# Kernel optimization log

Hardware: AMD Instinct MI355X
Metric: run time of the kernel (lower is better)

## Reference

```python
import jax, jax.numpy as jnp
import numpy as np

B, S, E, H = 2, 2048, 1024, 16
D = E // H  # head_dim = 64


def setup_inputs() -> dict:
    key = jax.random.key(0)
    ks = jax.random.split(key, 6)
    scale = 1.0 / np.sqrt(E)
    x = jax.random.normal(ks[0], (B, S, E), dtype=jnp.float32)
    mask = jnp.ones((B, S), dtype=jnp.int32)
    Wqkv = jax.random.normal(ks[1], (E, 3 * E), dtype=jnp.float32) * scale
    bqkv = jax.random.normal(ks[2], (3 * E,), dtype=jnp.float32) * 0.01
    Wout = jax.random.normal(ks[3], (E, E), dtype=jnp.float32) * scale
    bout = jax.random.normal(ks[4], (E,), dtype=jnp.float32) * 0.01
    return {"x": x, "mask": mask, "Wqkv": Wqkv, "bqkv": bqkv, "Wout": Wout, "bout": bout}


def reference(x, mask, Wqkv, bqkv, Wout, bout):
    Bn, Sn, En = x.shape
    qkv = x @ Wqkv + bqkv                      # [B,S,3E]
    qkv = qkv.reshape(Bn, Sn, 3, H, D)
    qkv = jnp.transpose(qkv, (2, 0, 3, 1, 4))  # [3,B,H,S,D]
    q, k, v = qkv[0], qkv[1], qkv[2]
    scores = jnp.einsum('bhqd,bhkd->bhqk', q, k) / np.sqrt(D).astype(np.float32)
    m = mask[:, None, None, :]                 # [B,1,1,S]
    scores = jnp.where(m == 0, jnp.float32(-jnp.inf), scores)
    attn = jax.nn.softmax(scores, axis=-1)
    out = jnp.einsum('bhqk,bhkd->bhqd', attn, v)  # [B,H,S,D]
    out = jnp.transpose(out, (0, 2, 1, 3)).reshape(Bn, Sn, En)
    return out @ Wout + bout
```

## Files before the change

### kernel.cpp

```cpp
#include <hip/hip_runtime.h>


typedef __attribute__((ext_vector_type(8))) short short8;
typedef __attribute__((ext_vector_type(4))) float floatx4;
typedef unsigned short ushort_t;

static __device__ __forceinline__ ushort_t f2bf(float f) {
    unsigned u = __float_as_uint(f);
    u += 0x7fffu + ((u >> 16) & 1u);
    return (ushort_t)(u >> 16);
}
static __device__ __forceinline__ float bf2f(ushort_t h) {
    return __uint_as_float(((unsigned)h) << 16);
}
#if __has_builtin(__builtin_amdgcn_cvt_pk_bf16_f32)
typedef __attribute__((ext_vector_type(2))) __bf16 bf16x2_t;
static __device__ __forceinline__ unsigned pack2bf(float a, float b) {
    bf16x2_t r = __builtin_amdgcn_cvt_pk_bf16_f32(a, b);
    return __builtin_bit_cast(unsigned, r);
}
#else
static __device__ __forceinline__ unsigned pack2bf(float a, float b) {
    return (unsigned)f2bf(a) | ((unsigned)f2bf(b) << 16);
}
#endif
static __device__ __forceinline__ float hexp2(float x) {
    return __builtin_amdgcn_exp2f(x);
}
static __device__ __forceinline__ void gload16(const void* g, void* l) {
    __builtin_amdgcn_global_load_lds(
        (const __attribute__((address_space(1))) unsigned int*)g,
        (__attribute__((address_space(3))) unsigned int*)l, 16, 0, 0);
}

__global__ __launch_bounds__(256) void prep(
    const float* __restrict__ x, ushort_t* __restrict__ xb,
    const float* __restrict__ Wqkv, ushort_t* __restrict__ wqT,
    const float* __restrict__ Wout, ushort_t* __restrict__ woT,
    const int* __restrict__ mask, float* __restrict__ maddg)
{
    __shared__ float tile[32][33];
    const int bk = blockIdx.x;
    const int t = threadIdx.x;
    if (bk < 4096) {
        int i = bk * 256 + t;
        float4 v = ((const float4*)x)[i];
        uint2 o;
        o.x = pack2bf(v.x, v.y);
        o.y = pack2bf(v.z, v.w);
        ((uint2*)xb)[i] = o;
        return;
    }
    if (bk < 8192) {
        const float* W; ushort_t* WT; int K, N, id;
        if (bk < 7168) { W = Wqkv; WT = wqT; K = 1024; N = 3072; id = bk - 4096;
                         int nb = (id % 96) * 32, kb = (id / 96) * 32;
                         const int r = t >> 3, c4 = (t & 7) * 4;
                         float4 v = *(const float4*)&W[(size_t)(kb + r) * N + nb + c4];
                         tile[r][c4+0]=v.x; tile[r][c4+1]=v.y; tile[r][c4+2]=v.z; tile[r][c4+3]=v.w;
                         __syncthreads();
                         uint2 o;
                         o.x = pack2bf(tile[c4+0][r], tile[c4+1][r]);
                         o.y = pack2bf(tile[c4+2][r], tile[c4+3][r]);
                         ((uint2*)WT)[((size_t)(nb + r) * K + kb + c4) >> 2] = o;
        } else {         W = Wout; WT = woT; K = 1024; N = 1024; id = bk - 7168;
                         int nb = (id % 32) * 32, kb = (id / 32) * 32;
                         const int r = t >> 3, c4 = (t & 7) * 4;
                         float4 v = *(const float4*)&W[(size_t)(kb + r) * N + nb + c4];
                         tile[r][c4+0]=v.x; tile[r][c4+1]=v.y; tile[r][c4+2]=v.z; tile[r][c4+3]=v.w;
                         __syncthreads();
                         uint2 o;
                         o.x = pack2bf(tile[c4+0][r], tile[c4+1][r]);
                         o.y = pack2bf(tile[c4+2][r], tile[c4+3][r]);
                         ((uint2*)WT)[((size_t)(nb + r) * K + kb + c4) >> 2] = o;
        }
        return;
    }
    {
        int i = (bk - 8192) * 256 + t;
        maddg[i] = (mask[i] ? 0.f : -1e30f) - 24.0f;
    }
}

__global__ __launch_bounds__(256, 3) void gemm_qkv(
    const ushort_t* __restrict__ A, const ushort_t* __restrict__ B,
    const float* __restrict__ bias, ushort_t* __restrict__ qkvb,
    ushort_t* __restrict__ vtg)
{
    const int K = 1024;
    __shared__ ushort_t Ah[128][32], Bh[128][32];
    __shared__ ushort_t Tb[64][136];
    const int bn = blockIdx.x * 128, bm = blockIdx.y * 128;
    const int t = threadIdx.x, w = t >> 6, lane = t & 63;
    const int l15 = lane & 15, quad = lane >> 4;
    const int wm = w >> 1, wn = w & 1;

    const int srow = w * 32 + (lane >> 2);
    const int skp  = (lane & 3) ^ ((lane >> 2) & 3);
    const int scol = skp * 8;
    const ushort_t* ga = A + (size_t)(bm + srow) * K + scol;
    const ushort_t* gb = B + (size_t)(bn + srow) * K + scol;
    const size_t rstep = (size_t)16 * K;
    const int fcol = ((quad ^ (l15 & 3)) * 8);

    floatx4 acc[4][4];
    #pragma unroll
    for (int mt = 0; mt < 4; ++mt)
        #pragma unroll
        for (int nt = 0; nt < 4; ++nt) acc[mt][nt] = (floatx4){0.f, 0.f, 0.f, 0.f};

    for (int k0 = 0; k0 < K; k0 += 32) {
        #pragma unroll
        for (int i = 0; i < 2; ++i) {
            gload16(ga + i * rstep + k0, &Ah[w * 32 + i * 16][0]);
            gload16(gb + i * rstep + k0, &Bh[w * 32 + i * 16][0]);
        }
        __syncthreads();
        short8 ah[4], bh[4];
        #pragma unroll
        for (int x = 0; x < 4; ++x) {
            ah[x] = *(const short8*)&Ah[wm * 64 + x * 16 + l15][fcol];
            bh[x] = *(const short8*)&Bh[wn * 64 + x * 16 + l15][fcol];
        }
        #pragma unroll
        for (int mt = 0; mt < 4; ++mt)
            #pragma unroll
            for (int nt = 0; nt < 4; ++nt)
                acc[mt][nt] = __builtin_amdgcn_mfma_f32_16x16x32_bf16(ah[mt], bh[nt], acc[mt][nt], 0, 0, 0);
        __syncthreads();
    }

    if (bn < 2048) {
        #pragma unroll
        for (int mt = 0; mt < 4; ++mt)
            #pragma unroll
            for (int r = 0; r < 4; ++r) {
                size_t row = (size_t)(bm + wm * 64 + mt * 16 + quad * 4 + r) * 2048;
                #pragma unroll
                for (int nt = 0; nt < 4; ++nt) {
                    int col = bn + wn * 64 + nt * 16 + l15;
                    qkvb[row + col] = f2bf(acc[mt][nt][r] + bias[col]);
                }
            }
    } else {
        const int h0 = (bn - 2048) >> 6;
        const int b  = bm >> 11, s0 = bm & 2047;
        #pragma unroll
        for (int hh = 0; hh < 2; ++hh) {
            if (wn == hh) {
                #pragma unroll
                for (int mt = 0; mt < 4; ++mt)
                    #pragma unroll
                    for (int nt = 0; nt < 4; ++nt) {
                        int d = nt * 16 + l15;
                        int sb = wm * 64 + mt * 16 + quad * 4;
                        float bv = bias[bn + hh * 64 + nt * 16 + l15];
                        uint2 pk;
                        pk.x = pack2bf(acc[mt][nt][0] + bv, acc[mt][nt][1] + bv);
                        pk.y = pack2bf(acc[mt][nt][2] + bv, acc[mt][nt][3] + bv);
                        *(uint2*)&Tb[d][sb] = pk;
                    }
            }
            __syncthreads();
            ushort_t* vbase = vtg + ((size_t)((b * 16 + h0 + hh) * 64)) * 2048 + s0;
            #pragma unroll
            for (int it = 0; it < 4; ++it) {
                int idx = t + it * 256;
                int d = idx >> 4, ch = idx & 15;
                uint4 v = *(const uint4*)&Tb[d][ch * 8];
                *(uint4*)&vbase[(size_t)d * 2048 + ch * 8] = v;
            }
            __syncthreads();
        }
    }
}

__global__ __launch_bounds__(256, 3) void gemm_bf16_f32_64(
    const ushort_t* __restrict__ A, const ushort_t* __restrict__ B,
    const float* __restrict__ bias, float* __restrict__ C,
    int M, int N, int K)
{
    __shared__ ushort_t Ah[64][32], Bh[128][32];
    const int bn = blockIdx.x * 128, bm = blockIdx.y * 64;
    const int t = threadIdx.x, w = t >> 6, lane = t & 63;
    const int l15 = lane & 15, quad = lane >> 4;
    const int wm = w >> 1, wn = w & 1;

    const int srow = w * 16 + (lane >> 2);
    const int skp  = (lane & 3) ^ ((lane >> 2) & 3);
    const int scol = skp * 8;
    const ushort_t* ga  = A + (size_t)(bm + srow) * K + scol;
    const ushort_t* gb0 = B + (size_t)(bn + srow) * K + scol;
    const ushort_t* gb1 = B + (size_t)(bn + 64 + srow) * K + scol;
    const int fcol = ((quad ^ (l15 & 3)) * 8);

    floatx4 acc[2][4];
    #pragma unroll
    for (int mt = 0; mt < 2; ++mt)
        #pragma unroll
        for (int nt = 0; nt < 4; ++nt) acc[mt][nt] = (floatx4){0.f, 0.f, 0.f, 0.f};

    for (int k0 = 0; k0 < K; k0 += 32) {
        gload16(ga  + k0, &Ah[w * 16][0]);
        gload16(gb0 + k0, &Bh[w * 16][0]);
        gload16(gb1 + k0, &Bh[64 + w * 16][0]);
        __syncthreads();
        short8 ah[2], bh[4];
        #pragma unroll
        for (int x = 0; x < 2; ++x)
            ah[x] = *(const short8*)&Ah[wm * 32 + x * 16 + l15][fcol];
        #pragma unroll
        for (int x = 0; x < 4; ++x)
            bh[x] = *(const short8*)&Bh[wn * 64 + x * 16 + l15][fcol];
        #pragma unroll
        for (int mt = 0; mt < 2; ++mt)
            #pragma unroll
            for (int nt = 0; nt < 4; ++nt)
                acc[mt][nt] = __builtin_amdgcn_mfma_f32_16x16x32_bf16(ah[mt], bh[nt], acc[mt][nt], 0, 0, 0);
        __syncthreads();
    }
    #pragma unroll
    for (int mt = 0; mt < 2; ++mt)
        #pragma unroll
        for (int r = 0; r < 4; ++r) {
            size_t row = (size_t)(bm + wm * 32 + mt * 16 + quad * 4 + r) * N;
            #pragma unroll
            for (int nt = 0; nt < 4; ++nt) {
                int col = bn + wn * 64 + nt * 16 + l15;
                C[row + col] = acc[mt][nt][r] + bias[col];
            }
        }
}

__global__ __launch_bounds__(256, 2) void flash_v6(
    const ushort_t* __restrict__ qkv, const ushort_t* __restrict__ vtg,
    const float* __restrict__ maddg, ushort_t* __restrict__ attn)
{
    __shared__ ushort_t Ks[2][64][64];
    __shared__ ushort_t Vt[2][64][64];
    __shared__ ushort_t Ps[4][2][16][72];
    __shared__ float MaddL[2048];

    const int blk = blockIdx.x;
    const int xcd = blk & 7, rr = blk >> 3;
    const int qi = rr & 15, g = xcd + 8 * (rr >> 4);
    const int b = g >> 4, h = g & 15, q0 = qi * 128;

    const int t = threadIdx.x, wave = t >> 6, lane = t & 63;
    const int l15 = lane & 15, quad = lane >> 4;
    const size_t bS = (size_t)b * 2048;
    const float c1 = 0.125f * 1.44269504088896340736f;

    short8 qf[2][2];
    #pragma unroll
    for (int tt = 0; tt < 2; ++tt) {
        int q = q0 + wave * 32 + tt * 16 + l15;
        const ushort_t* qp = qkv + (bS + q) * 2048 + h * 64;
        qf[tt][0] = *(const short8*)(qp + quad * 8);
        qf[tt][1] = *(const short8*)(qp + 32 + quad * 8);
    }

    const int srow  = wave * 16 + (lane >> 3);
    const int schnk = ((lane & 7) ^ ((lane >> 3) & 7)) * 8;
    const ushort_t* gK = qkv + (bS + srow) * 2048 + 1024 + h * 64 + schnk;
    const ushort_t* gV = vtg + ((size_t)(b * 16 + h) * 64 + srow) * 2048 + schnk;

    gload16(gK,            &Ks[0][wave * 16][0]);
    gload16(gK + 8 * 2048, &Ks[0][wave * 16 + 8][0]);
    gload16(gV,            &Vt[0][wave * 16][0]);
    gload16(gV + 8 * 2048, &Vt[0][wave * 16 + 8][0]);
    {
        const float* gM = maddg + b * 2048 + wave * 512 + lane * 4;
        gload16(gM,       &MaddL[wave * 512]);
        gload16(gM + 256, &MaddL[wave * 512 + 256]);
    }
    __syncthreads();

    floatx4 outacc[2][4];
    float lsum[2] = {0.f, 0.f};
    #pragma unroll
    for (int tt = 0; tt < 2; ++tt)
        #pragma unroll
        for (int dt = 0; dt < 4; ++dt) outacc[tt][dt] = (floatx4){0.f, 0.f, 0.f, 0.f};

    int cur = 0;
    for (int kt = 0; kt < 32; ++kt) {
        const int k0 = kt * 64;
        {
            const int kn = (kt + 1 < 32) ? (kt + 1) * 64 : 0;
            const int nb = cur ^ 1;
            gload16(gK + (size_t)kn * 2048,            &Ks[nb][wave * 16][0]);
            gload16(gK + (size_t)(kn + 8) * 2048,      &Ks[nb][wave * 16 + 8][0]);
            gload16(gV + kn,                           &Vt[nb][wave * 16][0]);
            gload16(gV + kn + 8 * 2048,                &Vt[nb][wave * 16 + 8][0]);
        }

        short8 kf[2][4], vf[2][4];
        #pragma unroll
        for (int kc = 0; kc < 2; ++kc)
            #pragma unroll
            for (int c = 0; c < 4; ++c) {
                int ch = ((kc * 4 + quad) ^ (l15 & 7)) * 8;
                kf[kc][c] = *(const short8*)&Ks[cur][c * 16 + l15][ch];
                vf[kc][c] = *(const short8*)&Vt[cur][c * 16 + l15][ch];
            }
        float4 madd4[4];
        #pragma unroll
        for (int c = 0; c < 4; ++c)
            madd4[c] = *(const float4*)&MaddL[k0 + c * 16 + quad * 4];

        #pragma unroll
        for (int tt = 0; tt < 2; ++tt) {
            floatx4 sc[4];
            #pragma unroll
            for (int c = 0; c < 4; ++c) {
                sc[c] = (floatx4){0.f, 0.f, 0.f, 0.f};
                sc[c] = __builtin_amdgcn_mfma_f32_16x16x32_bf16(kf[0][c], qf[tt][0], sc[c], 0, 0, 0);
                sc[c] = __builtin_amdgcn_mfma_f32_16x16x32_bf16(kf[1][c], qf[tt][1], sc[c], 0, 0, 0);
            }
            #pragma unroll
            for (int c = 0; c < 4; ++c) {
                float p0 = hexp2(fmaf(sc[c][0], c1, madd4[c].x));
                float p1 = hexp2(fmaf(sc[c][1], c1, madd4[c].y));
                float p2 = hexp2(fmaf(sc[c][2], c1, madd4[c].z));
                float p3 = hexp2(fmaf(sc[c][3], c1, madd4[c].w));
                lsum[tt] += (p0 + p1) + (p2 + p3);
                uint2 pk;
                pk.x = pack2bf(p0, p1);
                pk.y = pack2bf(p2, p3);
                *(uint2*)&Ps[wave][tt][l15][c * 16 + quad * 4] = pk;
            }
            short8 pf0 = *(const short8*)&Ps[wave][tt][l15][quad * 8];
            short8 pf1 = *(const short8*)&Ps[wave][tt][l15][32 + quad * 8];
            #pragma unroll
            for (int dt = 0; dt < 4; ++dt) {
                outacc[tt][dt] = __builtin_amdgcn_mfma_f32_16x16x32_bf16(vf[0][dt], pf0, outacc[tt][dt], 0, 0, 0);
                outacc[tt][dt] = __builtin_amdgcn_mfma_f32_16x16x32_bf16(vf[1][dt], pf1, outacc[tt][dt], 0, 0, 0);
            }
        }
        __syncthreads();
        cur ^= 1;
    }

    #pragma unroll
    for (int tt = 0; tt < 2; ++tt) {
        lsum[tt] += __shfl_xor(lsum[tt], 16);
        lsum[tt] += __shfl_xor(lsum[tt], 32);
        float inv = 1.f / lsum[tt];
        int q = q0 + wave * 32 + tt * 16 + l15;
        ushort_t* orow = attn + (bS + q) * 1024 + h * 64;
        #pragma unroll
        for (int dt = 0; dt < 4; ++dt) {
            uint2 pk;
            pk.x = pack2bf(outacc[tt][dt][0] * inv, outacc[tt][dt][1] * inv);
            pk.y = pack2bf(outacc[tt][dt][2] * inv, outacc[tt][dt][3] * inv);
            *(uint2*)&orow[dt * 16 + quad * 4] = pk;
        }
    }
}

extern "C" void kernel_launch(void* const* d_in, const int* in_sizes, int n_in,
                              void* d_out, int out_size, void* d_ws, size_t ws_size,
                              hipStream_t stream) {
    const float* x    = (const float*)d_in[0];
    const int*   mask = (const int*)  d_in[1];
    const float* Wqkv = (const float*)d_in[2];
    const float* bqkv = (const float*)d_in[3];
    const float* Wout = (const float*)d_in[4];
    const float* bout = (const float*)d_in[5];
    float* out = (float*)d_out;

    char* ws = (char*)d_ws;
    ushort_t* xb    = (ushort_t*)(ws);
    ushort_t* wqT   = (ushort_t*)(ws + 8388608);
    ushort_t* qkvb  = (ushort_t*)(ws + 14680064);
    ushort_t* vtg   = (ushort_t*)(ws + 31457280);
    ushort_t* attnb = (ushort_t*)(ws + 39845888);
    ushort_t* woT   = (ushort_t*)(ws + 48234496);
    float*    maddg = (float*)   (ws + 50331648);

    const int M = 4096, E = 1024, N3 = 3072;

    prep<<<dim3(8208), dim3(256), 0, stream>>>(
        x, xb, Wqkv, wqT, Wout, woT, mask, maddg);

    gemm_qkv<<<dim3(N3 / 128, M / 128), dim3(256), 0, stream>>>(
        xb, wqT, bqkv, qkvb, vtg);

    flash_v6<<<dim3(512), dim3(256), 0, stream>>>(qkvb, vtg, maddg, attnb);

    gemm_bf16_f32_64<<<dim3(E / 128, M / 64), dim3(256), 0, stream>>>(
        attnb, woT, bout, out, M, E, E);
}
```

Measured before the change: 201.7 us.

## Feed P directly from registers into 16x16x16 MFMA, drop LDS P staging

```diff
diff --git a/kernel.cpp b/kernel.cpp
--- a/kernel.cpp
+++ b/kernel.cpp
@@ -2,6 +2,7 @@
 
 
 typedef __attribute__((ext_vector_type(8))) short short8;
+typedef __attribute__((ext_vector_type(4))) short short4b;
 typedef __attribute__((ext_vector_type(4))) float floatx4;
 typedef unsigned short ushort_t;
 
@@ -31,6 +32,17 @@
     __builtin_amdgcn_global_load_lds(
         (const __attribute__((address_space(1))) unsigned int*)g,
         (__attribute__((address_space(3))) unsigned int*)l, 16, 0, 0);
+}
+
+static __device__ __forceinline__ floatx4 mfma16(short4b a, short4b b, floatx4 c) {
+#if __has_builtin(__builtin_amdgcn_mfma_f32_16x16x16_bf16)
+    return __builtin_amdgcn_mfma_f32_16x16x16_bf16(a, b, c, 0, 0, 0);
+#elif __has_builtin(__builtin_amdgcn_mfma_f32_16x16x16bf16_1k)
+    return __builtin_amdgcn_mfma_f32_16x16x16bf16_1k(a, b, c, 0, 0, 0);
+#else
+    asm("v_mfma_f32_16x16x16_bf16 %0, %1, %2, %0" : "+v"(c) : "v"(a), "v"(b));
+    return c;
+#endif
 }
 
 __global__ __launch_bounds__(256) void prep(
@@ -232,14 +244,12 @@
         }
 }
 
-__global__ __launch_bounds__(256, 2) void flash_v6(
+__global__ __launch_bounds__(256, 2) void flash_v7(
     const ushort_t* __restrict__ qkv, const ushort_t* __restrict__ vtg,
     const float* __restrict__ maddg, ushort_t* __restrict__ attn)
 {
     __shared__ ushort_t Ks[2][64][64];
     __shared__ ushort_t Vt[2][64][64];
-    __shared__ ushort_t Ps[4][2][16][72];
-    __shared__ float MaddL[2048];
 
     const int blk = blockIdx.x;
     const int xcd = blk & 7, rr = blk >> 3;
@@ -264,16 +274,12 @@
     const int schnk = ((lane & 7) ^ ((lane >> 3) & 7)) * 8;
     const ushort_t* gK = qkv + (bS + srow) * 2048 + 1024 + h * 64 + schnk;
     const ushort_t* gV = vtg + ((size_t)(b * 16 + h) * 64 + srow) * 2048 + schnk;
+    const float* gM = maddg + b * 2048;
 
     gload16(gK,            &Ks[0][wave * 16][0]);
     gload16(gK + 8 * 2048, &Ks[0][wave * 16 + 8][0]);
     gload16(gV,            &Vt[0][wave * 16][0]);
     gload16(gV + 8 * 2048, &Vt[0][wave * 16 + 8][0]);
-    {
-        const float* gM = maddg + b * 2048 + wave * 512 + lane * 4;
-        gload16(gM,       &MaddL[wave * 512]);
-        gload16(gM + 256, &MaddL[wave * 512 + 256]);
-    }
     __syncthreads();
 
     floatx4 outacc[2][4];
@@ -294,20 +300,27 @@
             gload16(gV + kn,                           &Vt[nb][wave * 16][0]);
             gload16(gV + kn + 8 * 2048,                &Vt[nb][wave * 16 + 8][0]);
         }
-
-        short8 kf[2][4], vf[2][4];
+        float4 madd4[4];
+        #pragma unroll
+        for (int c = 0; c < 4; ++c)
+            madd4[c] = *(const float4*)&gM[k0 + c * 16 + quad * 4];
+
+        short8 kf[2][4];
         #pragma unroll
         for (int kc = 0; kc < 2; ++kc)
             #pragma unroll
             for (int c = 0; c < 4; ++c) {
                 int ch = ((kc * 4 + quad) ^ (l15 & 7)) * 8;
                 kf[kc][c] = *(const short8*)&Ks[cur][c * 16 + l15][ch];
-                vf[kc][c] = *(const short8*)&Vt[cur][c * 16 + l15][ch];
-            }
-        float4 madd4[4];
-        #pragma unroll
-        for (int c = 0; c < 4; ++c)
-            madd4[c] = *(const float4*)&MaddL[k0 + c * 16 + quad * 4];
+            }
+        short4b vA[4][4];
+        #pragma unroll
+        for (int c = 0; c < 4; ++c) {
+            const int vby = (((2 * c + (quad >> 1)) ^ (l15 & 7)) * 16 + (quad & 1) * 8);
+            #pragma unroll
+            for (int dt = 0; dt < 4; ++dt)
+                vA[c][dt] = *(const short4b*)((const char*)&Vt[cur][dt * 16 + l15][0] + vby);
+        }
 
         #pragma unroll
         for (int tt = 0; tt < 2; ++tt) {
@@ -325,17 +338,13 @@
                 float p2 = hexp2(fmaf(sc[c][2], c1, madd4[c].z));
                 float p3 = hexp2(fmaf(sc[c][3], c1, madd4[c].w));
                 lsum[tt] += (p0 + p1) + (p2 + p3);
-                uint2 pk;
-                pk.x = pack2bf(p0, p1);
-                pk.y = pack2bf(p2, p3);
-                *(uint2*)&Ps[wave][tt][l15][c * 16 + quad * 4] = pk;
-            }
-            short8 pf0 = *(const short8*)&Ps[wave][tt][l15][quad * 8];
-            short8 pf1 = *(const short8*)&Ps[wave][tt][l15][32 + quad * 8];
-            #pragma unroll
-            for (int dt = 0; dt < 4; ++dt) {
-                outacc[tt][dt] = __builtin_amdgcn_mfma_f32_16x16x32_bf16(vf[0][dt], pf0, outacc[tt][dt], 0, 0, 0);
-                outacc[tt][dt] = __builtin_amdgcn_mfma_f32_16x16x32_bf16(vf[1][dt], pf1, outacc[tt][dt], 0, 0, 0);
+                uint2 u;
+                u.x = pack2bf(p0, p1);
+                u.y = pack2bf(p2, p3);
+                short4b pb = __builtin_bit_cast(short4b, u);
+                #pragma unroll
+                for (int dt = 0; dt < 4; ++dt)
+                    outacc[tt][dt] = mfma16(vA[c][dt], pb, outacc[tt][dt]);
             }
         }
         __syncthreads();
@@ -387,7 +396,7 @@
     gemm_qkv<<<dim3(N3 / 128, M / 128), dim3(256), 0, stream>>>(
         xb, wqT, bqkv, qkvb, vtg);
 
-    flash_v6<<<dim3(512), dim3(256), 0, stream>>>(qkvb, vtg, maddg, attnb);
+    flash_v7<<<dim3(512), dim3(256), 0, stream>>>(qkvb, vtg, maddg, attnb);
 
     gemm_bf16_f32_64<<<dim3(E / 128, M / 64), dim3(256), 0, stream>>>(
         attnb, woT, bout, out, M, E, E);
```

New measurement: 210.4 us. 1.04x slower.
